# Optimization experiments

Measured on AMD Instinct MI355X. Metric: run time of the kernel, lower is better.

## Reference

```python
import jax, jax.numpy as jnp
import numpy as np

N = 50000
NEG_SLOPE = 0.2
EPS = 1e-16


def add_self_loops(edge_index, n):
    loop = jnp.arange(n, dtype=edge_index.dtype)
    src = jnp.concatenate([edge_index[0], loop])
    dst = jnp.concatenate([edge_index[1], loop])
    return src, dst


def gat_conv(x, src, dst, W, att_src, att_dst, bias, n):
    # x: [N, F_in]; W: [F_in, H*D]; att_*: [H, D]; bias: [H*D]
    H, D = att_src.shape
    h = (x @ W).reshape(n, H, D)                      # [N, H, D]
    a_src = jnp.einsum('nhd,hd->nh', h, att_src)      # [N, H]
    a_dst = jnp.einsum('nhd,hd->nh', h, att_dst)
    e = jax.nn.leaky_relu(a_src[src] + a_dst[dst], NEG_SLOPE)  # [E, H]
    # softmax over incoming edges per destination node, per head
    m = jax.ops.segment_max(e, dst, num_segments=n)   # [N, H]
    ex = jnp.exp(e - m[dst])
    s = jax.ops.segment_sum(ex, dst, num_segments=n)
    alpha = ex / (s[dst] + EPS)                       # [E, H]
    msg = h[src] * alpha[:, :, None]                  # [E, H, D]
    out = jax.ops.segment_sum(msg, dst, num_segments=n)
    return out.reshape(n, H * D) + bias


def gcn_conv(x, src, dst, W, bias, n):
    h = x @ W                                         # [N, C]
    deg = jax.ops.segment_sum(jnp.ones_like(src, dtype=h.dtype), dst, num_segments=n)
    dinv = jnp.where(deg > 0, jax.lax.rsqrt(deg), 0.0)
    norm = dinv[src] * dinv[dst]                      # [E]
    out = jax.ops.segment_sum(h[src] * norm[:, None], dst, num_segments=n)
    return out + bias


def setup_inputs() -> dict:
    key = jax.random.key(0)
    ks = jax.random.split(key, 12)
    F_in, hid, heads, ncls = 128, 32, 8, 8
    d2 = hid // 2  # 16
    E = 500000
    x = jax.random.normal(ks[0], (N, F_in), dtype=jnp.float32)
    edge_index = jax.random.randint(ks[1], (2, E), 0, N, dtype=jnp.int32)
    sc = lambda k, sh: jax.random.normal(k, sh, dtype=jnp.float32) * 0.05
    return {
        'x': x, 'edge_index': edge_index,
        'W1': sc(ks[2], (F_in, heads * hid)),
        'att_src1': sc(ks[3], (heads, hid)), 'att_dst1': sc(ks[4], (heads, hid)),
        'b1': jnp.zeros((heads * hid,), jnp.float32),
        'W2': sc(ks[5], (heads * hid, heads * d2)),
        'att_src2': sc(ks[6], (heads, d2)), 'att_dst2': sc(ks[7], (heads, d2)),
        'b2': jnp.zeros((heads * d2,), jnp.float32),
        'Wg': sc(ks[8], (heads * d2, ncls)),
        'bg': jnp.zeros((ncls,), jnp.float32),
    }


def reference(x, edge_index, W1, att_src1, att_dst1, b1, W2, att_src2, att_dst2, b2, Wg, bg):
    src, dst = add_self_loops(edge_index, N)
    h = gat_conv(x, src, dst, W1, att_src1, att_dst1, b1, N)
    h = jax.nn.relu(h)
    h = gat_conv(h, src, dst, W2, att_src2, att_dst2, b2, N)
    h = jax.nn.relu(h)
    return gcn_conv(h, src, dst, Wg, bg, N)
```

## Files before the change

### kernel.cpp

```cpp
#include <hip/hip_runtime.h>
#include <hip/hip_bf16.h>


typedef __attribute__((ext_vector_type(8))) short bf16x8;
typedef __attribute__((ext_vector_type(4))) float f32x4;


__global__ __launch_bounds__(256) void zero_deg_kernel(int* __restrict__ deg, int n) {
    int i = blockIdx.x * 256 + threadIdx.x;
    if (i < n) deg[i] = 0;
}

__global__ __launch_bounds__(256) void hist_kernel(const int* __restrict__ ei, int E, int Etot,
                                                   int* __restrict__ deg) {
    int e = blockIdx.x * 256 + threadIdx.x;
    if (e >= Etot) return;
    int d = (e < E) ? ei[E + e] : (e - E);
    atomicAdd(&deg[d], 1);
}

__global__ __launch_bounds__(256) void scanA_kernel(const int* __restrict__ deg,
                                                    int* __restrict__ off,
                                                    int* __restrict__ bsum, int n) {
    __shared__ int buf[256];
    int t = threadIdx.x;
    int i = blockIdx.x * 256 + t;
    int v = (i < n) ? deg[i] : 0;
    buf[t] = v;
    __syncthreads();
    #pragma unroll
    for (int st = 1; st < 256; st <<= 1) {
        int x = (t >= st) ? buf[t - st] : 0;
        __syncthreads();
        buf[t] += x;
        __syncthreads();
    }
    if (i < n) off[i + 1] = buf[t];
    if (t == 255) bsum[blockIdx.x] = buf[255];
}

__global__ __launch_bounds__(256) void scanB_kernel(int* __restrict__ bsum, int nb) {
    __shared__ int buf[256];
    int t = threadIdx.x;
    int v = (t < nb) ? bsum[t] : 0;
    buf[t] = v;
    __syncthreads();
    #pragma unroll
    for (int st = 1; st < 256; st <<= 1) {
        int x = (t >= st) ? buf[t - st] : 0;
        __syncthreads();
        buf[t] += x;
        __syncthreads();
    }
    if (t < nb) bsum[t] = buf[t] - v;
}

__global__ __launch_bounds__(256) void scanC_kernel(const int* __restrict__ deg,
                                                    int* __restrict__ off,
                                                    const int* __restrict__ bsum,
                                                    int* __restrict__ cur,
                                                    float* __restrict__ dinv, int n) {
    int i = blockIdx.x * 256 + threadIdx.x;
    if (i < n) {
        int o = off[i + 1] + bsum[blockIdx.x];
        off[i + 1] = o;
        cur[i] = o - deg[i];
        dinv[i] = rsqrtf((float)deg[i]);
    }
    if (i == 0) off[0] = 0;
}

__global__ __launch_bounds__(256) void scatter_kernel(const int* __restrict__ ei, int E, int Etot,
                                                      int* __restrict__ cur,
                                                      int* __restrict__ ssrc) {
    int e = blockIdx.x * 256 + threadIdx.x;
    if (e >= Etot) return;
    int s, d;
    if (e < E) { s = ei[e]; d = ei[E + e]; }
    else       { s = e - E; d = e - E; }
    int pos = atomicAdd(&cur[d], 1);
    ssrc[pos] = s;
}


__device__ __forceinline__ float4 bf4_to_f4(uint2 v) {
    float4 r;
    r.x = __uint_as_float((v.x & 0xFFFFu) << 16);
    r.y = __uint_as_float(v.x & 0xFFFF0000u);
    r.z = __uint_as_float((v.y & 0xFFFFu) << 16);
    r.w = __uint_as_float(v.y & 0xFFFF0000u);
    return r;
}

__global__ __launch_bounds__(256) void cvt_bf16_kernel(const float* __restrict__ in,
                                                       ushort* __restrict__ outb, int count) {
    int i = (blockIdx.x * 256 + threadIdx.x) * 4;
    if (i >= count) return;
    float4 v = *reinterpret_cast<const float4*>(in + i);
    ushort4 u;
    __hip_bfloat16 b0 = __float2bfloat16(v.x); u.x = *reinterpret_cast<ushort*>(&b0);
    __hip_bfloat16 b1 = __float2bfloat16(v.y); u.y = *reinterpret_cast<ushort*>(&b1);
    __hip_bfloat16 b2 = __float2bfloat16(v.z); u.z = *reinterpret_cast<ushort*>(&b2);
    __hip_bfloat16 b3 = __float2bfloat16(v.w); u.w = *reinterpret_cast<ushort*>(&b3);
    *reinterpret_cast<ushort4*>(outb + i) = u;
}

template <int K, int NC>
__global__ __launch_bounds__(256) void wtrans_kernel(const float* __restrict__ W,
                                                     ushort* __restrict__ Wt) {
    int t = blockIdx.x * 256 + threadIdx.x;
    if (t >= K * NC) return;
    int nn = t / K, k = t % K;
    __hip_bfloat16 b = __float2bfloat16(W[(size_t)k * NC + nn]);
    Wt[t] = *reinterpret_cast<ushort*>(&b);
}


template <int K, int D>
__global__ __launch_bounds__(256) void wprep_kernel(const float* __restrict__ W,
                                                    const float* __restrict__ att_s,
                                                    const float* __restrict__ att_d,
                                                    float* __restrict__ ws,
                                                    float* __restrict__ wd) {
    int t = blockIdx.x * 256 + threadIdx.x;
    if (t >= K * 8) return;
    int k = t >> 3, h = t & 7;
    const float* wrow = W + (size_t)k * (8 * D) + h * D;
    const float* as = att_s + h * D;
    const float* ad = att_d + h * D;
    float s1 = 0.f, s2 = 0.f;
    #pragma unroll
    for (int d = 0; d < D; d += 4) {
        float4 wv = *reinterpret_cast<const float4*>(wrow + d);
        float4 av = *reinterpret_cast<const float4*>(as + d);
        float4 dv = *reinterpret_cast<const float4*>(ad + d);
        s1 += wv.x * av.x + wv.y * av.y + wv.z * av.z + wv.w * av.w;
        s2 += wv.x * dv.x + wv.y * dv.y + wv.z * dv.z + wv.w * dv.w;
    }
    ws[t] = s1;
    wd[t] = s2;
}

template <int K>
__global__ __launch_bounds__(256) void adots_kernel(const ushort* __restrict__ Xb,
                                                    const float* __restrict__ ws,
                                                    const float* __restrict__ wd,
                                                    float* __restrict__ a_s,
                                                    float* __restrict__ a_d, int n) {
    int gid = blockIdx.x * 256 + threadIdx.x;
    if (gid >= n * 8) return;
    int node = gid >> 3, h = gid & 7;
    const ushort* xp = Xb + (size_t)node * K;
    float s1 = 0.f, s2 = 0.f;
    #pragma unroll 4
    for (int k = 0; k < K; k += 8) {
        uint4 v = *reinterpret_cast<const uint4*>(xp + k);
        float4 x0 = bf4_to_f4(make_uint2(v.x, v.y));
        float4 x1 = bf4_to_f4(make_uint2(v.z, v.w));
        s1 += x0.x * ws[(k + 0) * 8 + h] + x0.y * ws[(k + 1) * 8 + h] +
              x0.z * ws[(k + 2) * 8 + h] + x0.w * ws[(k + 3) * 8 + h] +
              x1.x * ws[(k + 4) * 8 + h] + x1.y * ws[(k + 5) * 8 + h] +
              x1.z * ws[(k + 6) * 8 + h] + x1.w * ws[(k + 7) * 8 + h];
        s2 += x0.x * wd[(k + 0) * 8 + h] + x0.y * wd[(k + 1) * 8 + h] +
              x0.z * wd[(k + 2) * 8 + h] + x0.w * wd[(k + 3) * 8 + h] +
              x1.x * wd[(k + 4) * 8 + h] + x1.y * wd[(k + 5) * 8 + h] +
              x1.z * wd[(k + 6) * 8 + h] + x1.w * wd[(k + 7) * 8 + h];
    }
    a_s[gid] = s1;
    a_d[gid] = s2;
}


template <int K, int NC, int BN>
__global__ __launch_bounds__(256) void mfma_gemm_kernel(const ushort* __restrict__ Ab,
                                                        const ushort* __restrict__ Bt,
                                                        ushort* __restrict__ Cb, int M) {
    constexpr int BM = 128, BK = 32;
    constexpr int FN = BN / 32;
    __shared__ ushort As[BM * BK];
    __shared__ ushort Bs[BN * BK];
    const int tid = threadIdx.x;
    const int lane = tid & 63;
    const int wid = tid >> 6;
    const int bm = blockIdx.y * BM;
    const int bn = blockIdx.x * BN;
    const int wm = (wid >> 1) * 64;
    const int wn = (wid & 1) * (BN / 2);
    const int l15 = lane & 15;
    const int l4 = lane >> 4;
    f32x4 zero4 = {0.f, 0.f, 0.f, 0.f};
    f32x4 acc[4][FN];
    #pragma unroll
    for (int i = 0; i < 4; ++i)
        #pragma unroll
        for (int j = 0; j < FN; ++j) acc[i][j] = zero4;

    for (int k0 = 0; k0 < K; k0 += BK) {
        #pragma unroll
        for (int p = 0; p < 2; ++p) {
            int ci = tid + p * 256;
            int r = ci >> 2, c = ci & 3;
            int row = bm + r;
            uint4 v = make_uint4(0, 0, 0, 0);
            if (row < M) v = *reinterpret_cast<const uint4*>(&Ab[(size_t)row * K + k0 + c * 8]);
            *reinterpret_cast<uint4*>(&As[r * BK + c * 8]) = v;
        }
        #pragma unroll
        for (int p = 0; p < BN / 64; ++p) {
            int ci = tid + p * 256;
            int r = ci >> 2, c = ci & 3;
            uint4 v = *reinterpret_cast<const uint4*>(&Bt[(size_t)(bn + r) * K + k0 + c * 8]);
            *reinterpret_cast<uint4*>(&Bs[r * BK + c * 8]) = v;
        }
        __syncthreads();
        bf16x8 af[4], bfr[FN];
        #pragma unroll
        for (int i = 0; i < 4; ++i)
            af[i] = *reinterpret_cast<const bf16x8*>(&As[(wm + 16 * i + l15) * BK + l4 * 8]);
        #pragma unroll
        for (int j = 0; j < FN; ++j)
            bfr[j] = *reinterpret_cast<const bf16x8*>(&Bs[(wn + 16 * j + l15) * BK + l4 * 8]);
        #pragma unroll
        for (int i = 0; i < 4; ++i)
            #pragma unroll
            for (int j = 0; j < FN; ++j)
                acc[i][j] = __builtin_amdgcn_mfma_f32_16x16x32_bf16(af[i], bfr[j], acc[i][j], 0, 0, 0);
        __syncthreads();
    }
    #pragma unroll
    for (int i = 0; i < 4; ++i) {
        #pragma unroll
        for (int p = 0; p < 4; ++p) {
            int row = bm + wm + 16 * i + l4 * 4 + p;
            if (row < M) {
                #pragma unroll
                for (int j = 0; j < FN; ++j) {
                    __hip_bfloat16 hb = __float2bfloat16(acc[i][j][p]);
                    Cb[(size_t)row * NC + bn + wn + 16 * j + l15] = *reinterpret_cast<ushort*>(&hb);
                }
            }
        }
    }
}


#define LRELU_EXP(e) __expf((e) > 0.f ? (e) : 0.2f * (e))

template <int C, int DH>
__global__ __launch_bounds__(256) void gat_agg_kernel(const ushort* __restrict__ hfeat,
                                                      const float* __restrict__ a_src,
                                                      const float* __restrict__ a_dst,
                                                      const int* __restrict__ off,
                                                      const int* __restrict__ ssrc,
                                                      const float* __restrict__ bias,
                                                      ushort* __restrict__ outb, int n) {
    constexpr int LPN = C / 4;
    constexpr int GS = DH / 4;
    const int node = blockIdx.x * (256 / LPN) + threadIdx.x / LPN;
    if (node >= n) return;
    const int local = threadIdx.x & (LPN - 1);
    const int c0 = local * 4;
    const int h = c0 / DH;
    const int subl = local & (GS - 1);
    const float adst = a_dst[node * 8 + h];
    const int o0 = off[node], o1 = off[node + 1];
    float ax = 0.f, ay = 0.f, az = 0.f, aw = 0.f, ssum = 0.f;
    int i = o0;
    const int nfull = o0 + ((o1 - o0) / GS) * GS;
    for (; i < nfull; i += GS) {
        int smy = ssrc[i + subl];
        float e = a_src[smy * 8 + h] + adst;
        float evmy = LRELU_EXP(e);
        int sj[GS];
        #pragma unroll
        for (int j = 0; j < GS; ++j) sj[j] = __shfl(smy, j, GS);
        uint2 rv[GS];
        #pragma unroll
        for (int j = 0; j < GS; ++j)
            rv[j] = *reinterpret_cast<const uint2*>(&hfeat[(size_t)sj[j] * C + c0]);
        #pragma unroll
        for (int j = 0; j < GS; ++j) {
            float ev = __shfl(evmy, j, GS);
            float4 hv = bf4_to_f4(rv[j]);
            ssum += ev;
            ax += ev * hv.x; ay += ev * hv.y; az += ev * hv.z; aw += ev * hv.w;
        }
    }
    for (; i < o1; ++i) {
        int s = ssrc[i];
        float e = a_src[s * 8 + h] + adst;
        float v = LRELU_EXP(e);
        uint2 rvv = *reinterpret_cast<const uint2*>(&hfeat[(size_t)s * C + c0]);
        float4 hv = bf4_to_f4(rvv);
        ssum += v;
        ax += v * hv.x; ay += v * hv.y; az += v * hv.z; aw += v * hv.w;
    }
    float sinv = 1.f / (ssum + 1e-16f);
    float4 bb = *reinterpret_cast<const float4*>(bias + c0);
    float ox = fmaxf(ax * sinv + bb.x, 0.f);
    float oy = fmaxf(ay * sinv + bb.y, 0.f);
    float oz = fmaxf(az * sinv + bb.z, 0.f);
    float ow = fmaxf(aw * sinv + bb.w, 0.f);
    ushort4 u;
    __hip_bfloat16 b0 = __float2bfloat16(ox); u.x = *reinterpret_cast<ushort*>(&b0);
    __hip_bfloat16 b1 = __float2bfloat16(oy); u.y = *reinterpret_cast<ushort*>(&b1);
    __hip_bfloat16 b2 = __float2bfloat16(oz); u.z = *reinterpret_cast<ushort*>(&b2);
    __hip_bfloat16 b3 = __float2bfloat16(ow); u.w = *reinterpret_cast<ushort*>(&b3);
    *reinterpret_cast<ushort4*>(&outb[(size_t)node * C + c0]) = u;
}


__global__ __launch_bounds__(256) void gcn_gemm_kernel(const ushort* __restrict__ Ab,
                                                       const float* __restrict__ Wg,
                                                       float* __restrict__ g, int n) {
    __shared__ float W[128 * 8];
    for (int i = threadIdx.x; i < 1024; i += 256) W[i] = Wg[i];
    __syncthreads();
    int gid = blockIdx.x * 256 + threadIdx.x;
    if (gid >= n * 8) return;
    int node = gid >> 3, c = gid & 7;
    const ushort* ap = Ab + (size_t)node * 128;
    float acc = 0.f;
    #pragma unroll
    for (int k = 0; k < 128; k += 8) {
        uint4 v = *reinterpret_cast<const uint4*>(ap + k);
        float4 x0 = bf4_to_f4(make_uint2(v.x, v.y));
        float4 x1 = bf4_to_f4(make_uint2(v.z, v.w));
        acc += x0.x * W[(k + 0) * 8 + c] + x0.y * W[(k + 1) * 8 + c] +
               x0.z * W[(k + 2) * 8 + c] + x0.w * W[(k + 3) * 8 + c] +
               x1.x * W[(k + 4) * 8 + c] + x1.y * W[(k + 5) * 8 + c] +
               x1.z * W[(k + 6) * 8 + c] + x1.w * W[(k + 7) * 8 + c];
    }
    g[gid] = acc;
}

__global__ __launch_bounds__(256) void gcn_agg_kernel(const float* __restrict__ g,
                                                      const float* __restrict__ dinv,
                                                      const int* __restrict__ off,
                                                      const int* __restrict__ ssrc,
                                                      const float* __restrict__ bg,
                                                      float* __restrict__ outp, int n) {
    int gid = blockIdx.x * 256 + threadIdx.x;
    if (gid >= n * 8) return;
    int node = gid >> 3, c = gid & 7;
    int o0 = off[node], o1 = off[node + 1];
    float acc = 0.f;
    for (int i = o0; i < o1; ++i) {
        int s = ssrc[i];
        acc += g[(size_t)s * 8 + c] * dinv[s];
    }
    outp[gid] = acc * dinv[node] + bg[c];
}


extern "C" void kernel_launch(void* const* d_in, const int* in_sizes, int n_in,
                              void* d_out, int out_size, void* d_ws, size_t ws_size,
                              hipStream_t stream) {
    const float* x      = (const float*)d_in[0];
    const int*   ei     = (const int*)d_in[1];
    const float* W1     = (const float*)d_in[2];
    const float* att_s1 = (const float*)d_in[3];
    const float* att_d1 = (const float*)d_in[4];
    const float* b1     = (const float*)d_in[5];
    const float* W2     = (const float*)d_in[6];
    const float* att_s2 = (const float*)d_in[7];
    const float* att_d2 = (const float*)d_in[8];
    const float* b2     = (const float*)d_in[9];
    const float* Wg     = (const float*)d_in[10];
    const float* bg     = (const float*)d_in[11];
    float* out = (float*)d_out;

    const int n    = in_sizes[0] / 128;
    const int E    = in_sizes[1] / 2;
    const int Etot = E + n;

    float*  wsp   = (float*)d_ws;
    float*  regA  = wsp;
    float*  regB  = regA + (size_t)n * 128;
    float*  regC  = regB + (size_t)n * 128;
    float*  a_s   = regC + (size_t)n * 64;
    float*  a_d   = a_s + (size_t)n * 8;
    float*  g     = a_d + (size_t)n * 8;
    float*  dinv  = g + (size_t)n * 8;
    float*  w1s   = dinv + n;
    float*  w1d   = w1s + 1024;
    float*  w2s   = w1d + 1024;
    float*  w2d   = w2s + 2048;
    float*  w1t_f = w2d + 2048;
    float*  w2t_f = w1t_f + 16384;
    int*    off   = (int*)(w2t_f + 16384);
    int*    deg   = off + (n + 1);
    int*    cur   = deg + n;
    int*    ssrc  = cur + n;
    int*    bsum  = ssrc + Etot;

    ushort* h1b   = (ushort*)regA;
    ushort* out2b = (ushort*)regA;
    ushort* out1b = (ushort*)regB;
    ushort* xb    = (ushort*)regC;
    ushort* h2b   = (ushort*)regC;
    ushort* W1t   = (ushort*)w1t_f;
    ushort* W2t   = (ushort*)w2t_f;

    const dim3 b256(256);
    const int nch = (n + 255) / 256;

    zero_deg_kernel<<<nch, b256, 0, stream>>>(deg, n);
    hist_kernel<<<(Etot + 255) / 256, b256, 0, stream>>>(ei, E, Etot, deg);
    scanA_kernel<<<nch, b256, 0, stream>>>(deg, off, bsum, n);
    scanB_kernel<<<1, b256, 0, stream>>>(bsum, nch);
    scanC_kernel<<<nch, b256, 0, stream>>>(deg, off, bsum, cur, dinv, n);
    scatter_kernel<<<(Etot + 255) / 256, b256, 0, stream>>>(ei, E, Etot, cur, ssrc);

    wprep_kernel<128, 32><<<4, b256, 0, stream>>>(W1, att_s1, att_d1, w1s, w1d);
    wprep_kernel<256, 16><<<8, b256, 0, stream>>>(W2, att_s2, att_d2, w2s, w2d);
    cvt_bf16_kernel<<<(n * 128 / 4 + 255) / 256, b256, 0, stream>>>(x, xb, n * 128);
    wtrans_kernel<128, 256><<<(32768 + 255) / 256, b256, 0, stream>>>(W1, W1t);
    wtrans_kernel<256, 128><<<(32768 + 255) / 256, b256, 0, stream>>>(W2, W2t);

    adots_kernel<128><<<(n * 8 + 255) / 256, b256, 0, stream>>>(xb, w1s, w1d, a_s, a_d, n);
    mfma_gemm_kernel<128, 256, 128><<<dim3(2, (n + 127) / 128), b256, 0, stream>>>(xb, W1t, h1b, n);
    gat_agg_kernel<256, 32><<<(n + 3) / 4, b256, 0, stream>>>(h1b, a_s, a_d, off, ssrc, b1, out1b, n);

    adots_kernel<256><<<(n * 8 + 255) / 256, b256, 0, stream>>>(out1b, w2s, w2d, a_s, a_d, n);
    mfma_gemm_kernel<256, 128, 64><<<dim3(2, (n + 127) / 128), b256, 0, stream>>>(out1b, W2t, h2b, n);
    gat_agg_kernel<128, 16><<<(n + 7) / 8, b256, 0, stream>>>(h2b, a_s, a_d, off, ssrc, b2, out2b, n);

    gcn_gemm_kernel<<<(n * 8 + 255) / 256, b256, 0, stream>>>(out2b, Wg, g, n);
    gcn_agg_kernel<<<(n * 8 + 255) / 256, b256, 0, stream>>>(g, dinv, off, ssrc, bg, out, n);
}
```

Measured before the change: 263.3 us.

## Give each GAT node a full wavefront with split edges and 16-byte feature loads

The GAT aggregation now assigns one 64-lane wavefront per node. Lanes are split into edge groups, each lane loads 8 bf16 features with a 16-byte load, and the partial sums are combined with xor shuffles at the end. This replaces the older scheme of fewer lanes per node with shuffle-broadcast source indices and a scalar tail loop, to expose more memory-level parallelism for the gather. Separately, the GCN source-side dinv scaling moves into the GCN GEMM so the aggregation loop skips one gather per edge. In exchange, the shuffle reduction costs more and lanes go idle on low-degree nodes.

```diff
diff --git a/kernel.cpp b/kernel.cpp
--- a/kernel.cpp
+++ b/kernel.cpp
@@ -254,64 +254,64 @@
                                                       const int* __restrict__ ssrc,
                                                       const float* __restrict__ bias,
                                                       ushort* __restrict__ outb, int n) {
-    constexpr int LPN = C / 4;
-    constexpr int GS = DH / 4;
-    const int node = blockIdx.x * (256 / LPN) + threadIdx.x / LPN;
+    constexpr int LR = C / 8;
+    constexpr int EPS = 64 / LR;
+    const int node = blockIdx.x * 4 + (threadIdx.x >> 6);
     if (node >= n) return;
-    const int local = threadIdx.x & (LPN - 1);
-    const int c0 = local * 4;
+    const int lane = threadIdx.x & 63;
+    const int lir = lane & (LR - 1);
+    const int es = lane / LR;
+    const int c0 = lir * 8;
     const int h = c0 / DH;
-    const int subl = local & (GS - 1);
     const float adst = a_dst[node * 8 + h];
     const int o0 = off[node], o1 = off[node + 1];
-    float ax = 0.f, ay = 0.f, az = 0.f, aw = 0.f, ssum = 0.f;
-    int i = o0;
-    const int nfull = o0 + ((o1 - o0) / GS) * GS;
-    for (; i < nfull; i += GS) {
-        int smy = ssrc[i + subl];
-        float e = a_src[smy * 8 + h] + adst;
-        float evmy = LRELU_EXP(e);
-        int sj[GS];
-        #pragma unroll
-        for (int j = 0; j < GS; ++j) sj[j] = __shfl(smy, j, GS);
-        uint2 rv[GS];
-        #pragma unroll
-        for (int j = 0; j < GS; ++j)
-            rv[j] = *reinterpret_cast<const uint2*>(&hfeat[(size_t)sj[j] * C + c0]);
-        #pragma unroll
-        for (int j = 0; j < GS; ++j) {
-            float ev = __shfl(evmy, j, GS);
-            float4 hv = bf4_to_f4(rv[j]);
-            ssum += ev;
-            ax += ev * hv.x; ay += ev * hv.y; az += ev * hv.z; aw += ev * hv.w;
+    float a0 = 0.f, a1 = 0.f, a2 = 0.f, a3 = 0.f;
+    float a4 = 0.f, a5 = 0.f, a6 = 0.f, a7 = 0.f, ssum = 0.f;
+    #pragma unroll 4
+    for (int i = o0; i < o1; i += EPS) {
+        int idx = i + es;
+        bool ok = idx < o1;
+        int s = ssrc[ok ? idx : (o1 - 1)];
+        float e = a_src[s * 8 + h] + adst;
+        float ev = ok ? LRELU_EXP(e) : 0.f;
+        uint4 rv = *reinterpret_cast<const uint4*>(&hfeat[(size_t)s * C + c0]);
+        float4 x0 = bf4_to_f4(make_uint2(rv.x, rv.y));
+        float4 x1 = bf4_to_f4(make_uint2(rv.z, rv.w));
+        ssum += ev;
+        a0 += ev * x0.x; a1 += ev * x0.y; a2 += ev * x0.z; a3 += ev * x0.w;
+        a4 += ev * x1.x; a5 += ev * x1.y; a6 += ev * x1.z; a7 += ev * x1.w;
+    }
+    #pragma unroll
+    for (int m = LR; m < 64; m <<= 1) {
+        ssum += __shfl_xor(ssum, m);
+        a0 += __shfl_xor(a0, m); a1 += __shfl_xor(a1, m);
+        a2 += __shfl_xor(a2, m); a3 += __shfl_xor(a3, m);
+        a4 += __shfl_xor(a4, m); a5 += __shfl_xor(a5, m);
+        a6 += __shfl_xor(a6, m); a7 += __shfl_xor(a7, m);
+    }
+    if (es == 0) {
+        float sinv = 1.f / (ssum + 1e-16f);
+        float4 bb0 = *reinterpret_cast<const float4*>(bias + c0);
+        float4 bb1 = *reinterpret_cast<const float4*>(bias + c0 + 4);
+        float o[8];
+        o[0] = fmaxf(a0 * sinv + bb0.x, 0.f); o[1] = fmaxf(a1 * sinv + bb0.y, 0.f);
+        o[2] = fmaxf(a2 * sinv + bb0.z, 0.f); o[3] = fmaxf(a3 * sinv + bb0.w, 0.f);
+        o[4] = fmaxf(a4 * sinv + bb1.x, 0.f); o[5] = fmaxf(a5 * sinv + bb1.y, 0.f);
+        o[6] = fmaxf(a6 * sinv + bb1.z, 0.f); o[7] = fmaxf(a7 * sinv + bb1.w, 0.f);
+        ushort u[8];
+        #pragma unroll
+        for (int j = 0; j < 8; ++j) {
+            __hip_bfloat16 hb = __float2bfloat16(o[j]);
+            u[j] = *reinterpret_cast<ushort*>(&hb);
         }
-    }
-    for (; i < o1; ++i) {
-        int s = ssrc[i];
-        float e = a_src[s * 8 + h] + adst;
-        float v = LRELU_EXP(e);
-        uint2 rvv = *reinterpret_cast<const uint2*>(&hfeat[(size_t)s * C + c0]);
-        float4 hv = bf4_to_f4(rvv);
-        ssum += v;
-        ax += v * hv.x; ay += v * hv.y; az += v * hv.z; aw += v * hv.w;
-    }
-    float sinv = 1.f / (ssum + 1e-16f);
-    float4 bb = *reinterpret_cast<const float4*>(bias + c0);
-    float ox = fmaxf(ax * sinv + bb.x, 0.f);
-    float oy = fmaxf(ay * sinv + bb.y, 0.f);
-    float oz = fmaxf(az * sinv + bb.z, 0.f);
-    float ow = fmaxf(aw * sinv + bb.w, 0.f);
-    ushort4 u;
-    __hip_bfloat16 b0 = __float2bfloat16(ox); u.x = *reinterpret_cast<ushort*>(&b0);
-    __hip_bfloat16 b1 = __float2bfloat16(oy); u.y = *reinterpret_cast<ushort*>(&b1);
-    __hip_bfloat16 b2 = __float2bfloat16(oz); u.z = *reinterpret_cast<ushort*>(&b2);
-    __hip_bfloat16 b3 = __float2bfloat16(ow); u.w = *reinterpret_cast<ushort*>(&b3);
-    *reinterpret_cast<ushort4*>(&outb[(size_t)node * C + c0]) = u;
+        *reinterpret_cast<uint4*>(&outb[(size_t)node * C + c0]) = *reinterpret_cast<uint4*>(u);
+    }
 }
 
 
 __global__ __launch_bounds__(256) void gcn_gemm_kernel(const ushort* __restrict__ Ab,
                                                        const float* __restrict__ Wg,
+                                                       const float* __restrict__ dinv,
                                                        float* __restrict__ g, int n) {
     __shared__ float W[128 * 8];
     for (int i = threadIdx.x; i < 1024; i += 256) W[i] = Wg[i];
@@ -331,7 +331,7 @@
                x1.x * W[(k + 4) * 8 + c] + x1.y * W[(k + 5) * 8 + c] +
                x1.z * W[(k + 6) * 8 + c] + x1.w * W[(k + 7) * 8 + c];
     }
-    g[gid] = acc;
+    g[gid] = acc * dinv[node];
 }
 
 __global__ __launch_bounds__(256) void gcn_agg_kernel(const float* __restrict__ g,
@@ -347,7 +347,7 @@
     float acc = 0.f;
     for (int i = o0; i < o1; ++i) {
         int s = ssrc[i];
-        acc += g[(size_t)s * 8 + c] * dinv[s];
+        acc += g[(size_t)s * 8 + c];
     }
     outp[gid] = acc * dinv[node] + bg[c];
 }
@@ -424,8 +424,8 @@
 
     adots_kernel<256><<<(n * 8 + 255) / 256, b256, 0, stream>>>(out1b, w2s, w2d, a_s, a_d, n);
     mfma_gemm_kernel<256, 128, 64><<<dim3(2, (n + 127) / 128), b256, 0, stream>>>(out1b, W2t, h2b, n);
-    gat_agg_kernel<128, 16><<<(n + 7) / 8, b256, 0, stream>>>(h2b, a_s, a_d, off, ssrc, b2, out2b, n);
-
-    gcn_gemm_kernel<<<(n * 8 + 255) / 256, b256, 0, stream>>>(out2b, Wg, g, n);
+    gat_agg_kernel<128, 16><<<(n + 3) / 4, b256, 0, stream>>>(h2b, a_s, a_d, off, ssrc, b2, out2b, n);
+
+    gcn_gemm_kernel<<<(n * 8 + 255) / 256, b256, 0, stream>>>(out2b, Wg, dinv, g, n);
     gcn_agg_kernel<<<(n * 8 + 255) / 256, b256, 0, stream>>>(g, dinv, off, ssrc, bg, out, n);
 }
```

New measurement: 272.5 us. 1.03x slower.

## Merge prep kernels, fold scanB into scanC, prescale GCN features by dinv

Applied to the files above, without the earlier changes.

Replaces the zero, bf16-convert, weight-transpose and attention-weight-prep kernels with one grid-stride prep kernel. Fuses the degree histogram with the layer-1 attention-dot computation, and drops the single-block scanB by having each scanC block reduce the preceding block sums itself. Moves the source-side dinv multiply into the GCN GEMM so the aggregation loop no longer gathers dinv per edge. The aim is fewer launches and gathers, at the cost of redundant block-sum reductions in scanC and a fixed 2048-block grid-stride schedule.

```diff
diff --git a/kernel.cpp b/kernel.cpp
--- a/kernel.cpp
+++ b/kernel.cpp
@@ -6,18 +6,115 @@
 typedef __attribute__((ext_vector_type(4))) float f32x4;
 
 
-__global__ __launch_bounds__(256) void zero_deg_kernel(int* __restrict__ deg, int n) {
-    int i = blockIdx.x * 256 + threadIdx.x;
-    if (i < n) deg[i] = 0;
-}
-
-__global__ __launch_bounds__(256) void hist_kernel(const int* __restrict__ ei, int E, int Etot,
-                                                   int* __restrict__ deg) {
-    int e = blockIdx.x * 256 + threadIdx.x;
-    if (e >= Etot) return;
-    int d = (e < E) ? ei[E + e] : (e - E);
-    atomicAdd(&deg[d], 1);
-}
+__device__ __forceinline__ float4 bf4_to_f4(uint2 v) {
+    float4 r;
+    r.x = __uint_as_float((v.x & 0xFFFFu) << 16);
+    r.y = __uint_as_float(v.x & 0xFFFF0000u);
+    r.z = __uint_as_float((v.y & 0xFFFFu) << 16);
+    r.w = __uint_as_float(v.y & 0xFFFF0000u);
+    return r;
+}
+
+__device__ __forceinline__ ushort f_to_bf(float f) {
+    __hip_bfloat16 hb = __float2bfloat16(f);
+    return *reinterpret_cast<ushort*>(&hb);
+}
+
+
+__global__ __launch_bounds__(256) void prep_kernel(
+    const float* __restrict__ x,
+    const float* __restrict__ W1, const float* __restrict__ as1, const float* __restrict__ ad1,
+    const float* __restrict__ W2, const float* __restrict__ as2, const float* __restrict__ ad2,
+    ushort* __restrict__ xb, ushort* __restrict__ W1t, ushort* __restrict__ W2t,
+    float* __restrict__ w1s, float* __restrict__ w1d,
+    float* __restrict__ w2s, float* __restrict__ w2d,
+    int* __restrict__ deg, int n) {
+    const int tid = blockIdx.x * 256 + threadIdx.x;
+    const int NT = gridDim.x * 256;
+    for (int i = tid; i < n; i += NT) deg[i] = 0;
+    for (int j = tid; j < n * 32; j += NT) {
+        int i = j * 4;
+        float4 v = *reinterpret_cast<const float4*>(x + i);
+        ushort4 u = make_ushort4(f_to_bf(v.x), f_to_bf(v.y), f_to_bf(v.z), f_to_bf(v.w));
+        *reinterpret_cast<ushort4*>(xb + i) = u;
+    }
+    for (int j = tid; j < 32768; j += NT) {
+        int nn = j >> 7, k = j & 127;
+        W1t[j] = f_to_bf(W1[(size_t)k * 256 + nn]);
+    }
+    for (int j = tid; j < 32768; j += NT) {
+        int nn = j >> 8, k = j & 255;
+        W2t[j] = f_to_bf(W2[(size_t)k * 128 + nn]);
+    }
+    for (int j = tid; j < 1024; j += NT) {
+        int k = j >> 3, h = j & 7;
+        const float* wrow = W1 + (size_t)k * 256 + h * 32;
+        const float* as = as1 + h * 32;
+        const float* ad = ad1 + h * 32;
+        float s1 = 0.f, s2 = 0.f;
+        #pragma unroll
+        for (int d = 0; d < 32; d += 4) {
+            float4 wv = *reinterpret_cast<const float4*>(wrow + d);
+            float4 av = *reinterpret_cast<const float4*>(as + d);
+            float4 dv = *reinterpret_cast<const float4*>(ad + d);
+            s1 += wv.x * av.x + wv.y * av.y + wv.z * av.z + wv.w * av.w;
+            s2 += wv.x * dv.x + wv.y * dv.y + wv.z * dv.z + wv.w * dv.w;
+        }
+        w1s[j] = s1; w1d[j] = s2;
+    }
+    for (int j = tid; j < 2048; j += NT) {
+        int k = j >> 3, h = j & 7;
+        const float* wrow = W2 + (size_t)k * 128 + h * 16;
+        const float* as = as2 + h * 16;
+        const float* ad = ad2 + h * 16;
+        float s1 = 0.f, s2 = 0.f;
+        #pragma unroll
+        for (int d = 0; d < 16; d += 4) {
+            float4 wv = *reinterpret_cast<const float4*>(wrow + d);
+            float4 av = *reinterpret_cast<const float4*>(as + d);
+            float4 dv = *reinterpret_cast<const float4*>(ad + d);
+            s1 += wv.x * av.x + wv.y * av.y + wv.z * av.z + wv.w * av.w;
+            s2 += wv.x * dv.x + wv.y * dv.y + wv.z * dv.z + wv.w * dv.w;
+        }
+        w2s[j] = s1; w2d[j] = s2;
+    }
+}
+
+
+__global__ __launch_bounds__(256) void hist_adots_kernel(
+    const int* __restrict__ ei, int E, int Etot, int* __restrict__ deg,
+    const ushort* __restrict__ xb,
+    const float* __restrict__ w1s, const float* __restrict__ w1d,
+    float* __restrict__ a_s, float* __restrict__ a_d, int n) {
+    const int tid = blockIdx.x * 256 + threadIdx.x;
+    const int NT = gridDim.x * 256;
+    for (int e = tid; e < Etot; e += NT) {
+        int d = (e < E) ? ei[E + e] : (e - E);
+        atomicAdd(&deg[d], 1);
+    }
+    for (int j = tid; j < n * 8; j += NT) {
+        int node = j >> 3, h = j & 7;
+        const ushort* xp = xb + (size_t)node * 128;
+        float s1 = 0.f, s2 = 0.f;
+        #pragma unroll 4
+        for (int k = 0; k < 128; k += 8) {
+            uint4 v = *reinterpret_cast<const uint4*>(xp + k);
+            float4 x0 = bf4_to_f4(make_uint2(v.x, v.y));
+            float4 x1 = bf4_to_f4(make_uint2(v.z, v.w));
+            s1 += x0.x * w1s[(k + 0) * 8 + h] + x0.y * w1s[(k + 1) * 8 + h] +
+                  x0.z * w1s[(k + 2) * 8 + h] + x0.w * w1s[(k + 3) * 8 + h] +
+                  x1.x * w1s[(k + 4) * 8 + h] + x1.y * w1s[(k + 5) * 8 + h] +
+                  x1.z * w1s[(k + 6) * 8 + h] + x1.w * w1s[(k + 7) * 8 + h];
+            s2 += x0.x * w1d[(k + 0) * 8 + h] + x0.y * w1d[(k + 1) * 8 + h] +
+                  x0.z * w1d[(k + 2) * 8 + h] + x0.w * w1d[(k + 3) * 8 + h] +
+                  x1.x * w1d[(k + 4) * 8 + h] + x1.y * w1d[(k + 5) * 8 + h] +
+                  x1.z * w1d[(k + 6) * 8 + h] + x1.w * w1d[(k + 7) * 8 + h];
+        }
+        a_s[j] = s1;
+        a_d[j] = s2;
+    }
+}
+
 
 __global__ __launch_bounds__(256) void scanA_kernel(const int* __restrict__ deg,
                                                     int* __restrict__ off,
@@ -39,36 +136,34 @@
     if (t == 255) bsum[blockIdx.x] = buf[255];
 }
 
-__global__ __launch_bounds__(256) void scanB_kernel(int* __restrict__ bsum, int nb) {
-    __shared__ int buf[256];
-    int t = threadIdx.x;
-    int v = (t < nb) ? bsum[t] : 0;
-    buf[t] = v;
-    __syncthreads();
-    #pragma unroll
-    for (int st = 1; st < 256; st <<= 1) {
-        int x = (t >= st) ? buf[t - st] : 0;
-        __syncthreads();
-        buf[t] += x;
-        __syncthreads();
-    }
-    if (t < nb) bsum[t] = buf[t] - v;
-}
 
 __global__ __launch_bounds__(256) void scanC_kernel(const int* __restrict__ deg,
                                                     int* __restrict__ off,
                                                     const int* __restrict__ bsum,
                                                     int* __restrict__ cur,
                                                     float* __restrict__ dinv, int n) {
-    int i = blockIdx.x * 256 + threadIdx.x;
+    __shared__ int sred[256];
+    const int bid = blockIdx.x;
+    const int t = threadIdx.x;
+    sred[t] = (t < bid) ? bsum[t] : 0;
+    __syncthreads();
+    #pragma unroll
+    for (int st = 128; st > 0; st >>= 1) {
+        if (t < st) sred[t] += sred[t + st];
+        __syncthreads();
+    }
+    const int pre = sred[0];
+    int i = bid * 256 + t;
     if (i < n) {
-        int o = off[i + 1] + bsum[blockIdx.x];
+        int o = off[i + 1] + pre;
         off[i + 1] = o;
-        cur[i] = o - deg[i];
-        dinv[i] = rsqrtf((float)deg[i]);
+        int d = deg[i];
+        cur[i] = o - d;
+        dinv[i] = rsqrtf((float)d);
     }
     if (i == 0) off[0] = 0;
 }
+
 
 __global__ __launch_bounds__(256) void scatter_kernel(const int* __restrict__ ei, int E, int Etot,
                                                       int* __restrict__ cur,
@@ -82,64 +177,6 @@
     ssrc[pos] = s;
 }
 
-
-__device__ __forceinline__ float4 bf4_to_f4(uint2 v) {
-    float4 r;
-    r.x = __uint_as_float((v.x & 0xFFFFu) << 16);
-    r.y = __uint_as_float(v.x & 0xFFFF0000u);
-    r.z = __uint_as_float((v.y & 0xFFFFu) << 16);
-    r.w = __uint_as_float(v.y & 0xFFFF0000u);
-    return r;
-}
-
-__global__ __launch_bounds__(256) void cvt_bf16_kernel(const float* __restrict__ in,
-                                                       ushort* __restrict__ outb, int count) {
-    int i = (blockIdx.x * 256 + threadIdx.x) * 4;
-    if (i >= count) return;
-    float4 v = *reinterpret_cast<const float4*>(in + i);
-    ushort4 u;
-    __hip_bfloat16 b0 = __float2bfloat16(v.x); u.x = *reinterpret_cast<ushort*>(&b0);
-    __hip_bfloat16 b1 = __float2bfloat16(v.y); u.y = *reinterpret_cast<ushort*>(&b1);
-    __hip_bfloat16 b2 = __float2bfloat16(v.z); u.z = *reinterpret_cast<ushort*>(&b2);
-    __hip_bfloat16 b3 = __float2bfloat16(v.w); u.w = *reinterpret_cast<ushort*>(&b3);
-    *reinterpret_cast<ushort4*>(outb + i) = u;
-}
-
-template <int K, int NC>
-__global__ __launch_bounds__(256) void wtrans_kernel(const float* __restrict__ W,
-                                                     ushort* __restrict__ Wt) {
-    int t = blockIdx.x * 256 + threadIdx.x;
-    if (t >= K * NC) return;
-    int nn = t / K, k = t % K;
-    __hip_bfloat16 b = __float2bfloat16(W[(size_t)k * NC + nn]);
-    Wt[t] = *reinterpret_cast<ushort*>(&b);
-}
-
-
-template <int K, int D>
-__global__ __launch_bounds__(256) void wprep_kernel(const float* __restrict__ W,
-                                                    const float* __restrict__ att_s,
-                                                    const float* __restrict__ att_d,
-                                                    float* __restrict__ ws,
-                                                    float* __restrict__ wd) {
-    int t = blockIdx.x * 256 + threadIdx.x;
-    if (t >= K * 8) return;
-    int k = t >> 3, h = t & 7;
-    const float* wrow = W + (size_t)k * (8 * D) + h * D;
-    const float* as = att_s + h * D;
-    const float* ad = att_d + h * D;
-    float s1 = 0.f, s2 = 0.f;
-    #pragma unroll
-    for (int d = 0; d < D; d += 4) {
-        float4 wv = *reinterpret_cast<const float4*>(wrow + d);
-        float4 av = *reinterpret_cast<const float4*>(as + d);
-        float4 dv = *reinterpret_cast<const float4*>(ad + d);
-        s1 += wv.x * av.x + wv.y * av.y + wv.z * av.z + wv.w * av.w;
-        s2 += wv.x * dv.x + wv.y * dv.y + wv.z * dv.z + wv.w * dv.w;
-    }
-    ws[t] = s1;
-    wd[t] = s2;
-}
 
 template <int K>
 __global__ __launch_bounds__(256) void adots_kernel(const ushort* __restrict__ Xb,
@@ -235,8 +272,7 @@
             if (row < M) {
                 #pragma unroll
                 for (int j = 0; j < FN; ++j) {
-                    __hip_bfloat16 hb = __float2bfloat16(acc[i][j][p]);
-                    Cb[(size_t)row * NC + bn + wn + 16 * j + l15] = *reinterpret_cast<ushort*>(&hb);
+                    Cb[(size_t)row * NC + bn + wn + 16 * j + l15] = f_to_bf(acc[i][j][p]);
                 }
             }
         }
@@ -301,17 +337,14 @@
     float oy = fmaxf(ay * sinv + bb.y, 0.f);
     float oz = fmaxf(az * sinv + bb.z, 0.f);
     float ow = fmaxf(aw * sinv + bb.w, 0.f);
-    ushort4 u;
-    __hip_bfloat16 b0 = __float2bfloat16(ox); u.x = *reinterpret_cast<ushort*>(&b0);
-    __hip_bfloat16 b1 = __float2bfloat16(oy); u.y = *reinterpret_cast<ushort*>(&b1);
-    __hip_bfloat16 b2 = __float2bfloat16(oz); u.z = *reinterpret_cast<ushort*>(&b2);
-    __hip_bfloat16 b3 = __float2bfloat16(ow); u.w = *reinterpret_cast<ushort*>(&b3);
+    ushort4 u = make_ushort4(f_to_bf(ox), f_to_bf(oy), f_to_bf(oz), f_to_bf(ow));
     *reinterpret_cast<ushort4*>(&outb[(size_t)node * C + c0]) = u;
 }
 
 
 __global__ __launch_bounds__(256) void gcn_gemm_kernel(const ushort* __restrict__ Ab,
                                                        const float* __restrict__ Wg,
+                                                       const float* __restrict__ dinv,
                                                        float* __restrict__ g, int n) {
     __shared__ float W[128 * 8];
     for (int i = threadIdx.x; i < 1024; i += 256) W[i] = Wg[i];
@@ -331,7 +364,7 @@
                x1.x * W[(k + 4) * 8 + c] + x1.y * W[(k + 5) * 8 + c] +
                x1.z * W[(k + 6) * 8 + c] + x1.w * W[(k + 7) * 8 + c];
     }
-    g[gid] = acc;
+    g[gid] = acc * dinv[node];
 }
 
 __global__ __launch_bounds__(256) void gcn_agg_kernel(const float* __restrict__ g,
@@ -347,7 +380,7 @@
     float acc = 0.f;
     for (int i = o0; i < o1; ++i) {
         int s = ssrc[i];
-        acc += g[(size_t)s * 8 + c] * dinv[s];
+        acc += g[(size_t)s * 8 + c];
     }
     outp[gid] = acc * dinv[node] + bg[c];
 }
@@ -405,20 +438,13 @@
     const dim3 b256(256);
     const int nch = (n + 255) / 256;
 
-    zero_deg_kernel<<<nch, b256, 0, stream>>>(deg, n);
-    hist_kernel<<<(Etot + 255) / 256, b256, 0, stream>>>(ei, E, Etot, deg);
+    prep_kernel<<<2048, b256, 0, stream>>>(x, W1, att_s1, att_d1, W2, att_s2, att_d2,
+                                           xb, W1t, W2t, w1s, w1d, w2s, w2d, deg, n);
+    hist_adots_kernel<<<2048, b256, 0, stream>>>(ei, E, Etot, deg, xb, w1s, w1d, a_s, a_d, n);
     scanA_kernel<<<nch, b256, 0, stream>>>(deg, off, bsum, n);
-    scanB_kernel<<<1, b256, 0, stream>>>(bsum, nch);
     scanC_kernel<<<nch, b256, 0, stream>>>(deg, off, bsum, cur, dinv, n);
     scatter_kernel<<<(Etot + 255) / 256, b256, 0, stream>>>(ei, E, Etot, cur, ssrc);
 
-    wprep_kernel<128, 32><<<4, b256, 0, stream>>>(W1, att_s1, att_d1, w1s, w1d);
-    wprep_kernel<256, 16><<<8, b256, 0, stream>>>(W2, att_s2, att_d2, w2s, w2d);
-    cvt_bf16_kernel<<<(n * 128 / 4 + 255) / 256, b256, 0, stream>>>(x, xb, n * 128);
-    wtrans_kernel<128, 256><<<(32768 + 255) / 256, b256, 0, stream>>>(W1, W1t);
-    wtrans_kernel<256, 128><<<(32768 + 255) / 256, b256, 0, stream>>>(W2, W2t);
-
-    adots_kernel<128><<<(n * 8 + 255) / 256, b256, 0, stream>>>(xb, w1s, w1d, a_s, a_d, n);
     mfma_gemm_kernel<128, 256, 128><<<dim3(2, (n + 127) / 128), b256, 0, stream>>>(xb, W1t, h1b, n);
     gat_agg_kernel<256, 32><<<(n + 3) / 4, b256, 0, stream>>>(h1b, a_s, a_d, off, ssrc, b1, out1b, n);
 
@@ -426,6 +452,6 @@
     mfma_gemm_kernel<256, 128, 64><<<dim3(2, (n + 127) / 128), b256, 0, stream>>>(out1b, W2t, h2b, n);
     gat_agg_kernel<128, 16><<<(n + 7) / 8, b256, 0, stream>>>(h2b, a_s, a_d, off, ssrc, b2, out2b, n);
 
-    gcn_gemm_kernel<<<(n * 8 + 255) / 256, b256, 0, stream>>>(out2b, Wg, g, n);
+    gcn_gemm_kernel<<<(n * 8 + 255) / 256, b256, 0, stream>>>(out2b, Wg, dinv, g, n);
     gcn_agg_kernel<<<(n * 8 + 255) / 256, b256, 0, stream>>>(g, dinv, off, ssrc, bg, out, n);
 }
```

Result: faster. 241.1 us (-8.4%).
